# Kernel optimization log

Hardware: AMD Instinct MI355X
Metric: run time of the kernel (lower is better)

## Reference

```python
import jax, jax.numpy as jnp
import numpy as np

B, T, S, D, H, DK, DV = 4, 2048, 2048, 1024, 16, 64, 64


def setup_inputs() -> dict:
    key = jax.random.key(0)
    ks = jax.random.split(key, 12)
    sq = 1.0 / np.sqrt(D)
    return {
        "query": jax.random.normal(ks[0], (B, T, D), jnp.float32),
        "value": jax.random.normal(ks[1], (B, S, D), jnp.float32),
        "mask": jnp.ones((B, T, S), dtype=bool),
        "Wq": jax.random.normal(ks[2], (D, H, DK), jnp.float32) * sq,
        "bq": jnp.zeros((H, DK), jnp.float32),
        "Wk": jax.random.normal(ks[3], (D, H, DK), jnp.float32) * sq,
        "bk": jnp.zeros((H, DK), jnp.float32),
        "Wv": jax.random.normal(ks[4], (D, H, DV), jnp.float32) * sq,
        "bv": jnp.zeros((H, DV), jnp.float32),
        "Wo": jax.random.normal(ks[5], (H, DV, D), jnp.float32) * (1.0 / np.sqrt(H * DV)),
        "bo": jnp.zeros((D,), jnp.float32),
    }


def reference(query, value, mask, Wq, bq, Wk, bk, Wv, bv, Wo, bo):
    # key input defaults to value when only [query, value] is given
    q = jnp.einsum("btd,dhk->bthk", query, Wq) + bq  # [B,T,H,DK]
    k = jnp.einsum("bsd,dhk->bshk", value, Wk) + bk  # [B,S,H,DK]
    v = jnp.einsum("bsd,dhv->bshv", value, Wv) + bv  # [B,S,H,DV]
    # dot_product_equation 'aecd,abcd->acbe': scores[b,h,t,s]
    scores = jnp.einsum("bshk,bthk->bhts", k, q) * (1.0 / np.sqrt(DK))
    # MaskedSoftmax: mask [B,T,S] expanded at axis 1 -> [B,1,T,S]
    adder = (1.0 - mask[:, None, :, :].astype(scores.dtype)) * -10000.0
    probs = jax.nn.softmax(scores + adder, axis=-1)
    # combine_equation 'acbe,aecd->abcd'
    attn = jnp.einsum("bhts,bshv->bthv", probs, v)  # [B,T,H,DV]
    out = jnp.einsum("bthv,hvd->btd", attn, Wo) + bo  # [B,T,D]
    return out
```

## Files before the change

### kernel.cpp

```cpp
#include <hip/hip_runtime.h>

typedef __bf16 bf16x8 __attribute__((ext_vector_type(8)));
typedef __bf16 bf16x4 __attribute__((ext_vector_type(4)));
typedef float  f32x4  __attribute__((ext_vector_type(4)));
typedef int    i32x4  __attribute__((ext_vector_type(4)));

typedef __attribute__((address_space(1))) unsigned int as1_u32;
typedef __attribute__((address_space(3))) unsigned int as3_u32;

#define DEVI __device__ __forceinline__

DEVI unsigned short f2bf(float f) {
    union { float f; unsigned u; } v; v.f = f;
    unsigned r = (v.u + 0x7fffu + ((v.u >> 16) & 1u)) >> 16;
    return (unsigned short)r;
}

DEVI void gload16(const void* g, void* l) {
    __builtin_amdgcn_global_load_lds((const as1_u32*)g, (as3_u32*)l, 16, 0, 0);
}

#define C_EXP 0.18033688011112042f
#define MASK_ADD (-14426.950408889634f)

__global__ __launch_bounds__(256) void cvt_kernel(const float* __restrict__ in,
                                                  unsigned short* __restrict__ out,
                                                  int n8) {
    const int stride = gridDim.x * 256;
    for (int idx = blockIdx.x * 256 + threadIdx.x; idx < n8; idx += stride) {
        const f32x4 a = *(const f32x4*)(in + (size_t)idx * 8);
        const f32x4 b = *(const f32x4*)(in + (size_t)idx * 8 + 4);
        union { bf16x4 v[2]; i32x4 q; } u;
        u.v[0] = __builtin_convertvector(a, bf16x4);
        u.v[1] = __builtin_convertvector(b, bf16x4);
        *(i32x4*)(out + (size_t)idx * 8) = u.q;
    }
}

__global__ __launch_bounds__(256) void wtrans_kernel(const float* __restrict__ W0,
                                                     const float* __restrict__ W1,
                                                     const float* __restrict__ W2,
                                                     const float* __restrict__ W3,
                                                     unsigned short* __restrict__ T0,
                                                     unsigned short* __restrict__ T1,
                                                     unsigned short* __restrict__ T2,
                                                     unsigned short* __restrict__ T3) {
    __shared__ float tile[64][65];
    const float* W;
    unsigned short* WT;
    float scale = 1.0f;
    switch (blockIdx.z) {
        case 0:  W = W0; WT = T0; scale = C_EXP; break;
        case 1:  W = W1; WT = T1; break;
        case 2:  W = W2; WT = T2; break;
        default: W = W3; WT = T3; break;
    }
    const int k0 = blockIdx.x * 64, n0 = blockIdx.y * 64;
    const int i = threadIdx.x;
    const int c4 = (i & 15) * 4, rbase = i >> 4;
    for (int rr = 0; rr < 4; ++rr) {
        const int kl = rbase + rr * 16;
        const float4 v = *(const float4*)(W + (size_t)(k0 + kl) * 1024 + n0 + c4);
        tile[kl][c4 + 0] = v.x; tile[kl][c4 + 1] = v.y;
        tile[kl][c4 + 2] = v.z; tile[kl][c4 + 3] = v.w;
    }
    __syncthreads();
    for (int rr = 0; rr < 4; ++rr) {
        const int nl = rbase + rr * 16;
        ushort4 o;
        o.x = f2bf(tile[c4 + 0][nl] * scale); o.y = f2bf(tile[c4 + 1][nl] * scale);
        o.z = f2bf(tile[c4 + 2][nl] * scale); o.w = f2bf(tile[c4 + 3][nl] * scale);
        *(ushort4*)(WT + (size_t)(n0 + nl) * 1024 + k0 + c4) = o;
    }
}

__global__ __launch_bounds__(256) void maskflag_kernel(const int* __restrict__ mask,
                                                       unsigned* __restrict__ flagsW) {
    const int bid = blockIdx.x;
    const int b = bid >> 9, rem = bid & 511;
    const int tb = rem >> 5, si = rem & 31;
    const int i = threadIdx.x;
    const int t = tb * 128 + (i >> 1);
    const int s = si * 64 + (i & 1) * 32;
    const uint4* p = (const uint4*)(mask + ((size_t)(b * 2048 + t)) * 2048 + s);
    int ok = 1;
    #pragma unroll
    for (int u = 0; u < 8; ++u) {
        const uint4 a = p[u];
        ok &= (a.x != 0) & (a.y != 0) & (a.z != 0) & (a.w != 0);
    }
    int all = __syncthreads_and(ok);
    if (i == 0 && !all) atomicOr(&flagsW[b * 16 + tb], 1u << si);
}

template <int MODE>
__global__ __launch_bounds__(256) void mm_kernel(const unsigned short* __restrict__ A,
                                                 const unsigned short* __restrict__ BT,
                                                 const float* __restrict__ bias,
                                                 float bscale,
                                                 void* __restrict__ Ov) {
    __shared__ __align__(16) unsigned short Ab[128 * 32];
    __shared__ __align__(16) unsigned short Bb[128 * 32];
    const int bid = blockIdx.x;
    const int xcd = bid & 7, jj = bid >> 3;
    const int n0 = (jj & 7) * 128;
    const int m0 = ((jj >> 3) * 8 + xcd) * 128;
    const int i = threadIdx.x, w = i >> 6, l = i & 63;
    const int wm = w >> 1, wn = w & 1;
    const int c = l & 15, g = l >> 4;
    const int rloc = l >> 2;
    const int schunk = ((l & 3) ^ ((l >> 3) & 3)) * 8;
    const int rs = (c >> 1) & 3;

    f32x4 acc[4][4] = {};

    const unsigned short* Asrc = A + (size_t)(m0 + w * 32 + rloc) * 1024 + schunk;
    const unsigned short* Bsrc = BT + (size_t)(n0 + w * 32 + rloc) * 1024 + schunk;
    unsigned short* AbBase = &Ab[(w * 32) * 32];
    unsigned short* BbBase = &Bb[(w * 32) * 32];

    for (int k0 = 0; k0 < 1024; k0 += 32) {
        gload16(Asrc + k0,             AbBase);
        gload16(Asrc + k0 + 16 * 1024, AbBase + 16 * 32);
        gload16(Bsrc + k0,             BbBase);
        gload16(Bsrc + k0 + 16 * 1024, BbBase + 16 * 32);
        __syncthreads();
        bf16x8 af[4], bfr[4];
        #pragma unroll
        for (int mf = 0; mf < 4; ++mf)
            af[mf] = *(const bf16x8*)&Ab[(wm * 64 + mf * 16 + c) * 32 + (g ^ rs) * 8];
        #pragma unroll
        for (int nf = 0; nf < 4; ++nf)
            bfr[nf] = *(const bf16x8*)&Bb[(wn * 64 + nf * 16 + c) * 32 + (g ^ rs) * 8];
        #pragma unroll
        for (int mf = 0; mf < 4; ++mf)
            #pragma unroll
            for (int nf = 0; nf < 4; ++nf)
                acc[mf][nf] = __builtin_amdgcn_mfma_f32_16x16x32_bf16(af[mf], bfr[nf], acc[mf][nf], 0, 0, 0);
        __syncthreads();
    }

    #pragma unroll
    for (int nf = 0; nf < 4; ++nf) {
        const int n = n0 + wn * 64 + nf * 16 + c;
        const float bv = bias[n] * bscale;
        const int h = n >> 6, cc = n & 63;
        #pragma unroll
        for (int mf = 0; mf < 4; ++mf) {
            const int mbase = m0 + wm * 64 + mf * 16 + g * 4;
            if (MODE == 0) {
                const int b = mbase >> 11, t = mbase & 2047;
                unsigned short* O = (unsigned short*)Ov;
                #pragma unroll
                for (int r = 0; r < 4; ++r)
                    O[(((size_t)(b * 16 + h)) * 2048 + t + r) * 64 + cc] = f2bf(acc[mf][nf][r] + bv);
            } else if (MODE == 1) {
                const int b = mbase >> 11, t = mbase & 2047;
                f32x4 v;
                #pragma unroll
                for (int r = 0; r < 4; ++r) v[r] = acc[mf][nf][r] + bv;
                bf16x4 pv = __builtin_convertvector(v, bf16x4);
                unsigned short* O = (unsigned short*)Ov;
                *(bf16x4*)(O + (((size_t)(b * 16 + h)) * 64 + cc) * 2048 + t) = pv;
            } else {
                float* O = (float*)Ov;
                #pragma unroll
                for (int r = 0; r < 4; ++r)
                    O[(size_t)(mbase + r) * 1024 + n] = acc[mf][nf][r] + bv;
            }
        }
    }
}

__global__ __launch_bounds__(256, 4) void attn_kernel(const unsigned short* __restrict__ Qp,
                                                      const unsigned short* __restrict__ Kp,
                                                      const unsigned short* __restrict__ VTp,
                                                      const int* __restrict__ mask,
                                                      const unsigned* __restrict__ flagsW,
                                                      unsigned short* __restrict__ attnb) {
    __shared__ __align__(16) unsigned short Kt[2][64 * 64];
    __shared__ __align__(16) unsigned short Vt[2][64 * 64];

    const int bid = blockIdx.x;
    const int xcd = bid & 7, jj = bid >> 3;
    const int bh = xcd * 8 + (jj >> 4);
    const int tb = jj & 15;
    const int b = bh >> 4, h = bh & 15;
    const int i = threadIdx.x, w = i >> 6, l = i & 63;
    const int c = l & 15, g = l >> 4;

    const unsigned short* Qb  = Qp  + (size_t)bh * 2048 * 64;
    const unsigned short* Kb  = Kp  + (size_t)bh * 2048 * 64;
    const unsigned short* VTb = VTp + (size_t)bh * 64 * 2048;

    const int twave = tb * 128 + w * 32;
    const int tA = twave + c, tB = twave + 16 + c;

    const unsigned notall = __builtin_amdgcn_readfirstlane(flagsW[b * 16 + tb]);

    bf16x8 qfA[2], qfB[2];
    #pragma unroll
    for (int kq = 0; kq < 2; ++kq) {
        qfA[kq] = *(const bf16x8*)(Qb + (size_t)tA * 64 + kq * 32 + g * 8);
        qfB[kq] = *(const bf16x8*)(Qb + (size_t)tB * 64 + kq * 32 + g * 8);
    }

    f32x4 oA[4] = {}, oB[4] = {};
    f32x4 daccA = {}, daccB = {};
    const f32x4 zf = {};

    bf16x8 ones8;
    #pragma unroll
    for (int j = 0; j < 8; ++j) ones8[j] = (__bf16)1.0f;

    int rrow[4], rswz[4];
    #pragma unroll
    for (int sm = 0; sm < 4; ++sm) {
        rrow[sm] = (sm >> 1) * 32 + (c >> 2) * 8 + (sm & 1) * 4 + (c & 3);
        rswz[sm] = (rrow[sm] ^ (rrow[sm] >> 2)) & 7;
    }
    int vswz[4];
    #pragma unroll
    for (int vm = 0; vm < 4; ++vm) {
        const int rv = vm * 16 + c;
        vswz[vm] = (rv ^ (rv >> 2)) & 7;
    }

    const int srow = l >> 3, sslot = l & 7;

    const unsigned short* kstage[2];
    const unsigned short* vstage[2];
    #pragma unroll
    for (int u = 0; u < 2; ++u) {
        const int row = w * 16 + u * 8 + srow;
        const int ch = sslot ^ ((row ^ (row >> 2)) & 7);
        gload16(Kb + (size_t)row * 64 + ch * 8, &Kt[0][(w * 16 + u * 8) * 64]);
        gload16(VTb + (size_t)row * 2048 + ch * 8, &Vt[0][(w * 16 + u * 8) * 64]);
        kstage[u] = Kb + (size_t)(64 + row) * 64 + ch * 8;
        vstage[u] = VTb + (size_t)row * 2048 + 64 + ch * 8;
    }
    __syncthreads();

    #pragma unroll 2
    for (int it = 0; it < 32; ++it) {
        const int buf = it & 1;
        const int s0 = it * 64;

        if (it < 31) {
            #pragma unroll
            for (int u = 0; u < 2; ++u) {
                gload16(kstage[u], &Kt[buf ^ 1][(w * 16 + u * 8) * 64]);
                gload16(vstage[u], &Vt[buf ^ 1][(w * 16 + u * 8) * 64]);
                kstage[u] += 64 * 64;
                vstage[u] += 64;
            }
        }

        f32x4 scA[4], scB[4];
        __builtin_amdgcn_s_setprio(1);
        #pragma unroll
        for (int sm = 0; sm < 4; ++sm) {
            #pragma unroll
            for (int kq = 0; kq < 2; ++kq) {
                const bf16x8 kf = *(const bf16x8*)&Kt[buf][rrow[sm] * 64 + (((kq * 4 + g) ^ rswz[sm]) * 8)];
                if (kq == 0) {
                    scA[sm] = __builtin_amdgcn_mfma_f32_16x16x32_bf16(kf, qfA[0], zf, 0, 0, 0);
                    scB[sm] = __builtin_amdgcn_mfma_f32_16x16x32_bf16(kf, qfB[0], zf, 0, 0, 0);
                } else {
                    scA[sm] = __builtin_amdgcn_mfma_f32_16x16x32_bf16(kf, qfA[1], scA[sm], 0, 0, 0);
                    scB[sm] = __builtin_amdgcn_mfma_f32_16x16x32_bf16(kf, qfB[1], scB[sm], 0, 0, 0);
                }
            }
        }
        __builtin_amdgcn_s_setprio(0);

        if (notall & (1u << it)) {
            #pragma unroll
            for (int sm = 0; sm < 4; ++sm)
                #pragma unroll
                for (int r = 0; r < 4; ++r) {
                    const int s = s0 + (sm >> 1) * 32 + g * 8 + (sm & 1) * 4 + r;
                    if (mask[(size_t)(b * 2048 + tA) * 2048 + s] == 0) scA[sm][r] += MASK_ADD;
                    if (mask[(size_t)(b * 2048 + tB) * 2048 + s] == 0) scB[sm][r] += MASK_ADD;
                }
        }

        bf16x8 paA[2], paB[2];
        #pragma unroll
        for (int kv = 0; kv < 2; ++kv) {
            f32x4 a0, a1, b0, b1;
            #pragma unroll
            for (int r = 0; r < 4; ++r) {
                a0[r] = __builtin_amdgcn_exp2f(scA[kv * 2][r]);
                a1[r] = __builtin_amdgcn_exp2f(scA[kv * 2 + 1][r]);
                b0[r] = __builtin_amdgcn_exp2f(scB[kv * 2][r]);
                b1[r] = __builtin_amdgcn_exp2f(scB[kv * 2 + 1][r]);
            }
            union { struct { bf16x4 lo, hi; } hh; bf16x8 v; } ua, ub;
            ua.hh.lo = __builtin_convertvector(a0, bf16x4);
            ua.hh.hi = __builtin_convertvector(a1, bf16x4);
            ub.hh.lo = __builtin_convertvector(b0, bf16x4);
            ub.hh.hi = __builtin_convertvector(b1, bf16x4);
            paA[kv] = ua.v;
            paB[kv] = ub.v;
        }

        __builtin_amdgcn_s_setprio(1);
        #pragma unroll
        for (int kv = 0; kv < 2; ++kv) {
            daccA = __builtin_amdgcn_mfma_f32_16x16x32_bf16(ones8, paA[kv], daccA, 0, 0, 0);
            daccB = __builtin_amdgcn_mfma_f32_16x16x32_bf16(ones8, paB[kv], daccB, 0, 0, 0);
            #pragma unroll
            for (int vm = 0; vm < 4; ++vm) {
                const bf16x8 vf = *(const bf16x8*)&Vt[buf][(vm * 16 + c) * 64 + (((kv * 4 + g) ^ vswz[vm]) * 8)];
                oA[vm] = __builtin_amdgcn_mfma_f32_16x16x32_bf16(vf, paA[kv], oA[vm], 0, 0, 0);
                oB[vm] = __builtin_amdgcn_mfma_f32_16x16x32_bf16(vf, paB[kv], oB[vm], 0, 0, 0);
            }
        }
        __builtin_amdgcn_s_setprio(0);

        __syncthreads();
    }

    const float invA = 1.0f / daccA[0];
    const float invB = 1.0f / daccB[0];

    #pragma unroll
    for (int vm = 0; vm < 4; ++vm) {
        f32x4 vA, vB;
        #pragma unroll
        for (int r = 0; r < 4; ++r) { vA[r] = oA[vm][r] * invA; vB[r] = oB[vm][r] * invB; }
        bf16x4 pA = __builtin_convertvector(vA, bf16x4);
        bf16x4 pB = __builtin_convertvector(vB, bf16x4);
        *(bf16x4*)(attnb + (size_t)(b * 2048 + tA) * 1024 + h * 64 + vm * 16 + g * 4) = pA;
        *(bf16x4*)(attnb + (size_t)(b * 2048 + tB) * 1024 + h * 64 + vm * 16 + g * 4) = pB;
    }
}

extern "C" void kernel_launch(void* const* d_in, const int* in_sizes, int n_in,
                              void* d_out, int out_size, void* d_ws, size_t ws_size,
                              hipStream_t stream) {
    const float* query = (const float*)d_in[0];
    const float* value = (const float*)d_in[1];
    const int*   mask  = (const int*)d_in[2];
    const float* Wq = (const float*)d_in[3];
    const float* bq = (const float*)d_in[4];
    const float* Wk = (const float*)d_in[5];
    const float* bk = (const float*)d_in[6];
    const float* Wv = (const float*)d_in[7];
    const float* bv = (const float*)d_in[8];
    const float* Wo = (const float*)d_in[9];
    const float* bo = (const float*)d_in[10];

    char* ws = (char*)d_ws;
    unsigned short* WqT   = (unsigned short*)(ws + ((size_t)0  << 20));
    unsigned short* WkT   = (unsigned short*)(ws + ((size_t)2  << 20));
    unsigned short* WvT   = (unsigned short*)(ws + ((size_t)4  << 20));
    unsigned short* WoT   = (unsigned short*)(ws + ((size_t)6  << 20));
    unsigned*       flagsW= (unsigned*)      (ws + ((size_t)8  << 20));
    unsigned short* CONV  = (unsigned short*)(ws + ((size_t)9  << 20));
    unsigned short* Qp    = (unsigned short*)(ws + ((size_t)25 << 20));
    unsigned short* Kp    = (unsigned short*)(ws + ((size_t)41 << 20));
    unsigned short* VTp   = (unsigned short*)(ws + ((size_t)57 << 20));

    const int n8 = 8192 * 1024 / 8;

    hipMemsetAsync(flagsW, 0, 64 * sizeof(unsigned), stream);

    cvt_kernel<<<2048, 256, 0, stream>>>(value, CONV, n8);
    wtrans_kernel<<<dim3(16, 16, 4), 256, 0, stream>>>(Wq, Wk, Wv, Wo, WqT, WkT, WvT, WoT);
    maskflag_kernel<<<2048, 256, 0, stream>>>(mask, flagsW);
    mm_kernel<0><<<512, 256, 0, stream>>>(CONV, WkT, bk, 1.0f, Kp);
    mm_kernel<1><<<512, 256, 0, stream>>>(CONV, WvT, bv, 1.0f, VTp);

    cvt_kernel<<<2048, 256, 0, stream>>>(query, CONV, n8);
    mm_kernel<0><<<512, 256, 0, stream>>>(CONV, WqT, bq, C_EXP, Qp);

    attn_kernel<<<1024, 256, 0, stream>>>(Qp, Kp, VTp, mask, flagsW, CONV);

    mm_kernel<2><<<512, 256, 0, stream>>>(CONV, WoT, bo, 1.0f, (float*)d_out);
}
```

Before: 217.6 us.

## Double-buffer GEMM LDS tiles with wider K step and fuse K/V projections

The projection GEMM kernel now uses double-buffered LDS tiles with a K step of 64 instead of 32. The next tile is prefetched while MFMAs run on the current one, with a new XOR swizzle and s_setprio raised around the MFMA block. The K and V projections are merged into one launch over N=2048, relying on WkT and WvT sitting contiguously in the workspace, and the epilogue picks the output layout by column range. This is meant to hide global-load latency, halve the barriers, and cut one launch. In exchange, LDS use per block grows to 64 KB, which may lower occupancy.

```diff
diff --git a/kernel.cpp b/kernel.cpp
--- a/kernel.cpp
+++ b/kernel.cpp
@@ -93,77 +93,121 @@
     if (i == 0 && !all) atomicOr(&flagsW[b * 16 + tb], 1u << si);
 }
 
-template <int MODE>
+template <int MODE, int NB>
 __global__ __launch_bounds__(256) void mm_kernel(const unsigned short* __restrict__ A,
                                                  const unsigned short* __restrict__ BT,
-                                                 const float* __restrict__ bias,
+                                                 const float* __restrict__ biasK,
+                                                 const float* __restrict__ biasV,
                                                  float bscale,
-                                                 void* __restrict__ Ov) {
-    __shared__ __align__(16) unsigned short Ab[128 * 32];
-    __shared__ __align__(16) unsigned short Bb[128 * 32];
+                                                 void* __restrict__ OvK,
+                                                 void* __restrict__ OvV) {
+    __shared__ __align__(16) unsigned short Ab[2][128 * 64];
+    __shared__ __align__(16) unsigned short Bb[2][128 * 64];
     const int bid = blockIdx.x;
     const int xcd = bid & 7, jj = bid >> 3;
-    const int n0 = (jj & 7) * 128;
-    const int m0 = ((jj >> 3) * 8 + xcd) * 128;
+    const int n0 = (jj % NB) * 128;
+    const int m0 = ((jj / NB) * 8 + xcd) * 128;
     const int i = threadIdx.x, w = i >> 6, l = i & 63;
     const int wm = w >> 1, wn = w & 1;
     const int c = l & 15, g = l >> 4;
-    const int rloc = l >> 2;
-    const int schunk = ((l & 3) ^ ((l >> 3) & 3)) * 8;
-    const int rs = (c >> 1) & 3;
+    const int srow = l >> 3, sslot = l & 7;
 
     f32x4 acc[4][4] = {};
 
-    const unsigned short* Asrc = A + (size_t)(m0 + w * 32 + rloc) * 1024 + schunk;
-    const unsigned short* Bsrc = BT + (size_t)(n0 + w * 32 + rloc) * 1024 + schunk;
-    unsigned short* AbBase = &Ab[(w * 32) * 32];
-    unsigned short* BbBase = &Bb[(w * 32) * 32];
-
-    for (int k0 = 0; k0 < 1024; k0 += 32) {
-        gload16(Asrc + k0,             AbBase);
-        gload16(Asrc + k0 + 16 * 1024, AbBase + 16 * 32);
-        gload16(Bsrc + k0,             BbBase);
-        gload16(Bsrc + k0 + 16 * 1024, BbBase + 16 * 32);
-        __syncthreads();
-        bf16x8 af[4], bfr[4];
-        #pragma unroll
-        for (int mf = 0; mf < 4; ++mf)
-            af[mf] = *(const bf16x8*)&Ab[(wm * 64 + mf * 16 + c) * 32 + (g ^ rs) * 8];
-        #pragma unroll
-        for (int nf = 0; nf < 4; ++nf)
-            bfr[nf] = *(const bf16x8*)&Bb[(wn * 64 + nf * 16 + c) * 32 + (g ^ rs) * 8];
-        #pragma unroll
-        for (int mf = 0; mf < 4; ++mf)
-            #pragma unroll
-            for (int nf = 0; nf < 4; ++nf)
-                acc[mf][nf] = __builtin_amdgcn_mfma_f32_16x16x32_bf16(af[mf], bfr[nf], acc[mf][nf], 0, 0, 0);
+    const unsigned short* As[4];
+    const unsigned short* Bs[4];
+    unsigned lofs[4];
+    #pragma unroll
+    for (int u = 0; u < 4; ++u) {
+        const int rl = w * 32 + u * 8 + srow;
+        const int ch = sslot ^ ((rl ^ (rl >> 2)) & 7);
+        As[u] = A  + (size_t)(m0 + rl) * 1024 + ch * 8;
+        Bs[u] = BT + (size_t)(n0 + rl) * 1024 + ch * 8;
+        lofs[u] = (unsigned)((w * 32 + u * 8) * 64);
+    }
+
+    #pragma unroll
+    for (int u = 0; u < 4; ++u) {
+        gload16(As[u], &Ab[0][lofs[u]]);
+        gload16(Bs[u], &Bb[0][lofs[u]]);
+    }
+    __syncthreads();
+
+    int rsA[4], rsB[4];
+    #pragma unroll
+    for (int f = 0; f < 4; ++f) {
+        const int ra = wm * 64 + f * 16 + c;
+        const int rb = wn * 64 + f * 16 + c;
+        rsA[f] = (ra ^ (ra >> 2)) & 7;
+        rsB[f] = (rb ^ (rb >> 2)) & 7;
+    }
+
+    #pragma unroll 2
+    for (int it = 0; it < 16; ++it) {
+        const int buf = it & 1;
+        if (it < 15) {
+            #pragma unroll
+            for (int u = 0; u < 4; ++u) {
+                gload16(As[u] + (it + 1) * 64, &Ab[buf ^ 1][lofs[u]]);
+                gload16(Bs[u] + (it + 1) * 64, &Bb[buf ^ 1][lofs[u]]);
+            }
+        }
+        bf16x8 af[4][2], bfr[4][2];
+        #pragma unroll
+        for (int f = 0; f < 4; ++f)
+            #pragma unroll
+            for (int kk = 0; kk < 2; ++kk) {
+                af[f][kk]  = *(const bf16x8*)&Ab[buf][(wm * 64 + f * 16 + c) * 64 + (((kk * 4 + g) ^ rsA[f]) * 8)];
+                bfr[f][kk] = *(const bf16x8*)&Bb[buf][(wn * 64 + f * 16 + c) * 64 + (((kk * 4 + g) ^ rsB[f]) * 8)];
+            }
+        __builtin_amdgcn_s_setprio(1);
+        #pragma unroll
+        for (int kk = 0; kk < 2; ++kk)
+            #pragma unroll
+            for (int mf = 0; mf < 4; ++mf)
+                #pragma unroll
+                for (int nf = 0; nf < 4; ++nf)
+                    acc[mf][nf] = __builtin_amdgcn_mfma_f32_16x16x32_bf16(af[mf][kk], bfr[nf][kk], acc[mf][nf], 0, 0, 0);
+        __builtin_amdgcn_s_setprio(0);
         __syncthreads();
     }
 
     #pragma unroll
     for (int nf = 0; nf < 4; ++nf) {
         const int n = n0 + wn * 64 + nf * 16 + c;
-        const float bv = bias[n] * bscale;
-        const int h = n >> 6, cc = n & 63;
-        #pragma unroll
-        for (int mf = 0; mf < 4; ++mf) {
-            const int mbase = m0 + wm * 64 + mf * 16 + g * 4;
-            if (MODE == 0) {
+        if (MODE == 0 || (MODE == 3 && n0 < 1024)) {
+            const float bv = biasK[n] * bscale;
+            const int h = n >> 6, cc = n & 63;
+            unsigned short* O = (unsigned short*)OvK;
+            #pragma unroll
+            for (int mf = 0; mf < 4; ++mf) {
+                const int mbase = m0 + wm * 64 + mf * 16 + g * 4;
                 const int b = mbase >> 11, t = mbase & 2047;
-                unsigned short* O = (unsigned short*)Ov;
                 #pragma unroll
                 for (int r = 0; r < 4; ++r)
                     O[(((size_t)(b * 16 + h)) * 2048 + t + r) * 64 + cc] = f2bf(acc[mf][nf][r] + bv);
-            } else if (MODE == 1) {
+            }
+        } else if (MODE == 3) {
+            const int nn = n - 1024;
+            const float bv = biasV[nn];
+            const int h = nn >> 6, cc = nn & 63;
+            unsigned short* O = (unsigned short*)OvV;
+            #pragma unroll
+            for (int mf = 0; mf < 4; ++mf) {
+                const int mbase = m0 + wm * 64 + mf * 16 + g * 4;
                 const int b = mbase >> 11, t = mbase & 2047;
                 f32x4 v;
                 #pragma unroll
                 for (int r = 0; r < 4; ++r) v[r] = acc[mf][nf][r] + bv;
                 bf16x4 pv = __builtin_convertvector(v, bf16x4);
-                unsigned short* O = (unsigned short*)Ov;
                 *(bf16x4*)(O + (((size_t)(b * 16 + h)) * 64 + cc) * 2048 + t) = pv;
-            } else {
-                float* O = (float*)Ov;
+            }
+        } else {
+            const float bv = biasK[n] * bscale;
+            float* O = (float*)OvK;
+            #pragma unroll
+            for (int mf = 0; mf < 4; ++mf) {
+                const int mbase = m0 + wm * 64 + mf * 16 + g * 4;
                 #pragma unroll
                 for (int r = 0; r < 4; ++r)
                     O[(size_t)(mbase + r) * 1024 + n] = acc[mf][nf][r] + bv;
@@ -370,13 +414,12 @@
     cvt_kernel<<<2048, 256, 0, stream>>>(value, CONV, n8);
     wtrans_kernel<<<dim3(16, 16, 4), 256, 0, stream>>>(Wq, Wk, Wv, Wo, WqT, WkT, WvT, WoT);
     maskflag_kernel<<<2048, 256, 0, stream>>>(mask, flagsW);
-    mm_kernel<0><<<512, 256, 0, stream>>>(CONV, WkT, bk, 1.0f, Kp);
-    mm_kernel<1><<<512, 256, 0, stream>>>(CONV, WvT, bv, 1.0f, VTp);
+    mm_kernel<3, 16><<<1024, 256, 0, stream>>>(CONV, WkT, bk, bv, 1.0f, Kp, VTp);
 
     cvt_kernel<<<2048, 256, 0, stream>>>(query, CONV, n8);
-    mm_kernel<0><<<512, 256, 0, stream>>>(CONV, WqT, bq, C_EXP, Qp);
+    mm_kernel<0, 8><<<512, 256, 0, stream>>>(CONV, WqT, bq, bq, C_EXP, Qp, nullptr);
 
     attn_kernel<<<1024, 256, 0, stream>>>(Qp, Kp, VTp, mask, flagsW, CONV);
 
-    mm_kernel<2><<<512, 256, 0, stream>>>(CONV, WoT, bo, 1.0f, (float*)d_out);
-}
+    mm_kernel<2, 8><<<512, 256, 0, stream>>>(CONV, WoT, bo, bo, 1.0f, d_out, nullptr);
+}
```

Measured after the change: 204.5 us. -6.0%, faster.
